# Kernel tuning notes

Hardware: AMD Instinct MI355X
Metric: run time of the kernel (lower is better)

The kernel has to match this reference:

```python
import jax, jax.numpy as jnp
import numpy as np

CH_IN, CH_OUT, CH, NLAYERS = 40, 9, 64, 10
CH_CLOSE = 2 * CH
KSZ = 9  # stencil hard-coded to 9 in init_weights
H = 0.1


def conv1(X, Ker):
    # F.conv1d(X, Ker, padding=(k-1)//2); Ker: (Cout, Cin, k)
    pad = (Ker.shape[-1] - 1) // 2
    return jax.lax.conv_general_dilated(X, Ker, (1,), [(pad, pad)],
                                        dimension_numbers=('NCH', 'OIH', 'NCH'))


def conv1T(X, Ker):
    # F.conv_transpose1d(X, Ker, padding=(k-1)//2) with stride 1 ==
    # conv1d with swapped in/out channels and flipped taps, padding k-1-(k-1)//2
    k = Ker.shape[-1]
    pad = k - 1 - (k - 1) // 2
    Kt = jnp.flip(jnp.swapaxes(Ker, 0, 1), -1)
    return jax.lax.conv_general_dilated(X, Kt, (1,), [(pad, pad)],
                                        dimension_numbers=('NCH', 'OIH', 'NCH'))


def mean_masked(X, mask, axis, keepdims=False):
    return jnp.sum(X * mask, axis=axis, keepdims=keepdims) / jnp.sum(mask, axis=axis, keepdims=keepdims)


def tr2dist(Y):
    # pairwise distances of columns of Y (B,C,N) -> (B,N,N), per Pfold tr2DistSmall
    k = Y.shape[1]
    Z = Y - jnp.mean(Y, axis=2, keepdims=True)
    n2 = jnp.sum(Z * Z, axis=1)  # (B,N)
    D = n2[:, :, None] + n2[:, None, :] - 2.0 * jnp.einsum('bcn,bcm->bnm', Z, Z)
    D = 3.0 * D / k
    Dr = jnp.maximum(D, 0.0)
    safe = jnp.where(Dr > 0, Dr, 1.0)  # grad-safe sqrt
    return jnp.where(Dr > 0, jnp.sqrt(safe), 0.0)


def get_graph_lap(X, mask, sigma):
    # X: (B,C,N), mask: (B,1,N)
    mm = jnp.einsum('bci,bcj->bij', mask, mask)  # (B,N,N) pair mask
    msum = jnp.sum(mask, axis=2, keepdims=True)
    Xc = X - (jnp.sum(X * mask, axis=2, keepdims=True) / msum) * mask
    Xc = Xc / jnp.sqrt(jnp.sum(Xc * Xc, axis=2, keepdims=True) / msum + 1e-4)
    N = X.shape[2]
    pos = 0.5 * jnp.linspace(0.0, 1.0, N)[None, None, :] * mask  # (B,1,N)
    Xa = jnp.concatenate([Xc, pos], axis=1)
    W = tr2dist(Xa) * mm
    W = jnp.exp(-W / sigma * 10.0) * mm
    Wsum = jnp.sum(W, axis=1)  # (B,N)
    D = Wsum[:, :, None] * jnp.eye(N, dtype=W.dtype)  # diag(Wsum)
    L = D - W
    return 0.5 * (L + jnp.swapaxes(L, 1, 2)), W


def double_sym(Z, Wi, Bi, L, mask):
    A0 = conv1(Z + Bi[0], Wi[0]) * mask
    A0 = (A0 - mean_masked(A0, mask, 2, True)) * mask
    A0 = A0 / jnp.sqrt(jnp.sum(A0 * A0, axis=1, keepdims=True) + 1e-3)
    A1 = (conv1(Z + Bi[1], Wi[1]) @ L) * mask
    A1 = (A1 - mean_masked(A1, mask, 2, True)) * mask
    A1 = A1 / jnp.sqrt(jnp.sum(A1 * A1, axis=1, keepdims=True) + 1e-3)
    A0 = jax.nn.relu(A0)
    A1 = jax.nn.relu(A1)
    A0 = conv1T(A0, Wi[0]) * mask
    A1 = (conv1T(A1, Wi[1]) @ L) * mask
    return A0 + A1


def hypernet_forward(Z, mask, Kopen, Kclose, W, Bias):
    mask = mask[:, None, :]  # (B,1,N)
    Z = jnp.einsum('ci,bin->bcn', Kopen, Z) * mask
    L, _ = get_graph_lap(Z, mask, 10.0)
    for i in range(W.shape[0]):
        if i % 10 == 0:
            L, _ = get_graph_lap(Z, mask, 10.0)
        Z = Z - H * double_sym(Z, W[i], Bias[i], L, mask)
    Z = jnp.einsum('oc,bcn->bon', Kclose, Z) * mask
    dists = jnp.stack([tr2dist(Z[:, 3 * i:3 * i + 3, :]) for i in range(Z.shape[1] // 3)], axis=1)
    return dists, Z  # dists: (B, chan_out//3, N, N)


def setup_inputs() -> dict:
    key = jax.random.key(0)
    ks = jax.random.split(key, 5)
    B, N = 8, 1024
    Z = jax.random.normal(ks[0], (B, CH_IN, N), dtype=jnp.float32)
    mask = jnp.ones((B, N), dtype=jnp.float32)
    so = float(CH) / CH_IN
    Kopen = jax.random.uniform(ks[1], (CH, CH_IN), minval=-so, maxval=so, dtype=jnp.float32)
    sc = float(CH_OUT) / CH
    Kclose = jax.random.uniform(ks[2], (CH_OUT, CH), minval=-sc, maxval=sc, dtype=jnp.float32)
    W = jax.random.uniform(ks[3], (NLAYERS, 2, CH_CLOSE, CH, KSZ), minval=-0.1, maxval=0.1, dtype=jnp.float32)
    Bias = jax.random.uniform(ks[4], (NLAYERS, 2, CH, 1), dtype=jnp.float32) * 0.001
    return {"Z": Z, "mask": mask, "Kopen": Kopen, "Kclose": Kclose, "W": W, "Bias": Bias}


def reference(Z, mask, Kopen, Kclose, W, Bias):
    return hypernet_forward(Z, mask, Kopen, Kclose, W, Bias)
```

## Files before the change

### kernel.cpp

```cpp
#include <hip/hip_runtime.h>
#include <cstddef>

#define BB 8
#define NN 1024
#define CIN 40
#define CH 64
#define CC 128
#define COUT 9
#define KS 9
#define NL 10
#define HSTEP 0.1f
#define SKC 2
#define SKH 4

typedef __attribute__((ext_vector_type(8))) short bf16x8;
typedef __attribute__((ext_vector_type(4))) float f32x4;

__device__ __forceinline__ unsigned short f2bf(float f) {
    union { float f; unsigned u; } v;
    v.f = f;
    unsigned u = v.u;
    u += 0x7FFFu + ((u >> 16) & 1u);
    return (unsigned short)(u >> 16);
}
__device__ __forceinline__ float bf2f(unsigned short h) {
    union { unsigned u; float f; } v;
    v.u = ((unsigned)h) << 16;
    return v.f;
}

__device__ __forceinline__ size_t pk_addr(int lb, int row, int col, int R, int KDv) {
    int chunk = ((lb * (R / 32) + (row >> 5)) * (KDv / 32) + (col >> 5)) * 2 + ((row >> 4) & 1);
    int lane = ((col >> 3) & 3) * 16 + (row & 15);
    return ((size_t)chunk * 64 + lane) * 8 + (col & 7);
}

__device__ __forceinline__ float blockSum(float v, float* red) {
    int tid = threadIdx.x;
    red[tid] = v;
    __syncthreads();
    for (int s = 128; s > 0; s >>= 1) {
        if (tid < s) red[tid] += red[tid + s];
        __syncthreads();
    }
    float r = red[0];
    __syncthreads();
    return r;
}

__global__ __launch_bounds__(256) void k_zero(float* __restrict__ p, int n) {
    int i = blockIdx.x * 256 + threadIdx.x;
    if (i < n) p[i] = 0.f;
}

__global__ __launch_bounds__(256) void k_prep_wbf(const float* __restrict__ Win,
                                                  unsigned short* __restrict__ PKc_h,
                                                  unsigned short* __restrict__ PKc_l,
                                                  unsigned short* __restrict__ PKt_h,
                                                  unsigned short* __restrict__ PKt_l) {
    int idx = blockIdx.x * 256 + threadIdx.x;
    const int total = NL * 2 * CC * CH * KS;
    if (idx >= total) return;
    int k = idx % KS;
    int t = idx / KS;
    int i = t % CH;  t /= CH;
    int o = t % CC;  t /= CC;
    int lb = t;
    float v = Win[idx];
    unsigned short h = f2bf(v);
    unsigned short l = f2bf(v - bf2f(h));
    size_t ac = pk_addr(lb, o, k * 64 + i, CC, 576);
    size_t at = pk_addr(lb, i, (8 - k) * 128 + o, CH, 1152);
    PKc_h[ac] = h;
    PKc_l[ac] = l;
    PKt_h[at] = h;
    PKt_l[at] = l;
}

__global__ __launch_bounds__(256) void k_prep_bks(const float* __restrict__ Win,
                                                  const float* __restrict__ Bias,
                                                  float* __restrict__ bks) {
    int idx = blockIdx.x * 256 + threadIdx.x;
    const int total = NL * 2 * CC * KS;
    if (idx >= total) return;
    int k = idx % KS;
    int t = idx / KS;
    int o = t % CC;
    int lb = t / CC;
    float s = 0.f;
    for (int i = 0; i < CH; ++i)
        s += Win[(((size_t)lb * CC + o) * CH + i) * KS + k] * Bias[lb * CH + i];
    bks[idx] = s;
}

__global__ __launch_bounds__(256) void k_open(const float* __restrict__ Zin,
                                              const float* __restrict__ mask,
                                              const float* __restrict__ Kop,
                                              float* __restrict__ Zcur) {
    int n = blockIdx.x * 256 + threadIdx.x;
    int c = blockIdx.y, b = blockIdx.z;
    float acc = 0.f;
    for (int i = 0; i < CIN; ++i)
        acc += Kop[c * CIN + i] * Zin[((size_t)b * CIN + i) * NN + n];
    Zcur[((size_t)b * CH + c) * NN + n] = acc * mask[b * NN + n];
}

__global__ __launch_bounds__(256) void k_za(const float* __restrict__ Zcur,
                                            const float* __restrict__ mask,
                                            float* __restrict__ Za) {
    __shared__ float red[256];
    int c = blockIdx.x;
    int b = blockIdx.y;
    int tid = threadIdx.x;
    const float* m = mask + b * NN;
    float x[4], mv[4];
    if (c < CH) {
        const float* src = Zcur + ((size_t)b * CH + c) * NN;
#pragma unroll
        for (int j = 0; j < 4; ++j) { int n = tid * 4 + j; x[j] = src[n]; mv[j] = m[n]; }
    } else {
#pragma unroll
        for (int j = 0; j < 4; ++j) { int n = tid * 4 + j; mv[j] = m[n]; x[j] = 0.5f * ((float)n / 1023.f) * mv[j]; }
    }
    float sm = 0.f, sxm = 0.f;
#pragma unroll
    for (int j = 0; j < 4; ++j) { sm += mv[j]; sxm += x[j] * mv[j]; }
    float msum = blockSum(sm, red);
    float xm = blockSum(sxm, red);
    if (c < CH) {
        float mean = xm / msum;
        float ss = 0.f;
#pragma unroll
        for (int j = 0; j < 4; ++j) { x[j] -= mean * mv[j]; ss += x[j] * x[j]; }
        ss = blockSum(ss, red);
        float sc = rsqrtf(ss / msum + 1e-4f);
#pragma unroll
        for (int j = 0; j < 4; ++j) x[j] *= sc;
    }
    float ps = 0.f;
#pragma unroll
    for (int j = 0; j < 4; ++j) ps += x[j];
    float pm = blockSum(ps, red) / (float)NN;
    float* dst = Za + ((size_t)b * 65 + c) * NN;
#pragma unroll
    for (int j = 0; j < 4; ++j) dst[tid * 4 + j] = x[j] - pm;
}

__global__ __launch_bounds__(256) void k_gramW(const float* __restrict__ Za,
                                               const float* __restrict__ mask,
                                               unsigned short* __restrict__ Wpk,
                                               float* __restrict__ Wsum) {
    __shared__ float As[65][68];
    __shared__ float Bs2[65][68];
    __shared__ unsigned short wt[64][72];
    __shared__ float csred[16][64];
    __shared__ float n2is[64], n2js[64];
    int i0 = blockIdx.x * 64, j0 = blockIdx.y * 64, b = blockIdx.z;
    int tid = threadIdx.x;
    for (int e = tid; e < 65 * 64; e += 256) {
        int c = e >> 6, t = e & 63;
        const float* src = Za + ((size_t)b * 65 + c) * NN;
        As[c][t] = src[i0 + t];
        Bs2[c][t] = src[j0 + t];
    }
    __syncthreads();
    if (tid < 64) {
        float s = 0.f;
        for (int c = 0; c < 65; ++c) { float v = As[c][tid]; s += v * v; }
        n2is[tid] = s;
    } else if (tid < 128) {
        int t = tid - 64;
        float s = 0.f;
        for (int c = 0; c < 65; ++c) { float v = Bs2[c][t]; s += v * v; }
        n2js[t] = s;
    }
    __syncthreads();
    int tx = tid & 15, ty = tid >> 4;
    float acc[4][4] = {};
    for (int c = 0; c < 65; ++c) {
        float a[4];
#pragma unroll
        for (int q = 0; q < 4; ++q) a[q] = As[c][ty * 4 + q];
        float bv[4];
        *reinterpret_cast<float4*>(bv) = *reinterpret_cast<const float4*>(&Bs2[c][tx * 4]);
#pragma unroll
        for (int q = 0; q < 4; ++q)
#pragma unroll
            for (int r = 0; r < 4; ++r) acc[q][r] += a[q] * bv[r];
    }
    const float* m = mask + b * NN;
    float csacc[4] = {0.f, 0.f, 0.f, 0.f};
    for (int q = 0; q < 4; ++q) {
        int i = i0 + ty * 4 + q;
        float n2i = n2is[ty * 4 + q], mi = m[i];
#pragma unroll
        for (int r = 0; r < 4; ++r) {
            int j = j0 + tx * 4 + r;
            float D = n2i + n2js[tx * 4 + r] - 2.f * acc[q][r];
            D *= (3.f / 65.f);
            D = fmaxf(D, 0.f);
            float dist = (D > 0.f) ? sqrtf(D) : 0.f;
            float mmv = mi * m[j];
            float res = expf(-dist * mmv) * mmv;
            wt[ty * 4 + q][tx * 4 + r] = f2bf(res);
            csacc[r] += res;
        }
    }
#pragma unroll
    for (int r = 0; r < 4; ++r) csred[ty][tx * 4 + r] = csacc[r];
    __syncthreads();
    for (int s = 8; s > 0; s >>= 1) {
        if (ty < s) {
#pragma unroll
            for (int r = 0; r < 4; ++r) csred[ty][tx * 4 + r] += csred[ty + s][tx * 4 + r];
        }
        __syncthreads();
    }
    if (ty == 0) {
#pragma unroll
        for (int r = 0; r < 4; ++r)
            atomicAdd(&Wsum[b * NN + j0 + tx * 4 + r], csred[0][tx * 4 + r]);
    }
    for (int e = tid; e < 512; e += 256) {
        int li = e >> 3, ljb = (e & 7) * 8;
        int row = i0 + li, col = j0 + ljb;
        int chunk = ((b * 32 + (row >> 5)) * 32 + (col >> 5)) * 2 + ((row >> 4) & 1);
        int lane2 = ((col >> 3) & 3) * 16 + (row & 15);
        unsigned short* dp = Wpk + ((size_t)chunk * 64 + lane2) * 8;
        *reinterpret_cast<ushort4*>(dp) = *reinterpret_cast<ushort4*>(&wt[li][ljb]);
        *reinterpret_cast<ushort4*>(dp + 4) = *reinterpret_cast<ushort4*>(&wt[li][ljb + 4]);
    }
}

__global__ __launch_bounds__(256) void k_conv1_mfma(const float* __restrict__ Zcur,
                                                    const unsigned short* __restrict__ Wh,
                                                    const unsigned short* __restrict__ Wl,
                                                    const float* __restrict__ bksl,
                                                    const float* __restrict__ mask,
                                                    float* __restrict__ C0,
                                                    float* __restrict__ C1,
                                                    unsigned short* __restrict__ C1pk) {
    __shared__ __align__(16) unsigned short xh[80][64];
    __shared__ __align__(16) unsigned short xl[80][64];
    int n0 = blockIdx.x * 64;
    int y = blockIdx.y;
    int b = blockIdx.z;
    int br = y >> 1, half = y & 1;
    int tid = threadIdx.x;
    const float* Xb = Zcur + (size_t)b * CH * NN;

    for (int e = tid; e < 64 * 20; e += 256) {
        int i = e / 20, t = e - i * 20;
        int gn = n0 + t * 4 - 4;
        float4 v = make_float4(0.f, 0.f, 0.f, 0.f);
        if (gn >= 0 && gn + 3 < NN) v = *reinterpret_cast<const float4*>(&Xb[(size_t)i * NN + gn]);
        float vv[4] = {v.x, v.y, v.z, v.w};
#pragma unroll
        for (int j = 0; j < 4; ++j) {
            int row = t * 4 + j;
            int col = i ^ ((row & 7) << 3);
            unsigned short h = f2bf(vv[j]);
            xh[row][col] = h;
            xl[row][col] = f2bf(vv[j] - bf2f(h));
        }
    }
    __syncthreads();

    int wid = tid >> 6, lane = tid & 63;
    int wo = (wid >> 1) * 32, wn = (wid & 1) * 32;
    int r = lane & 15, g = lane >> 4;
    int r32 = half * 2 + (wid >> 1);
    size_t brOff = (size_t)br * (CC / 32) * (576 / 32) * 1024;

    f32x4 acc[2][2] = {};
#pragma unroll 3
    for (int q = 0; q < 18; ++q) {
        int k = q >> 1, s = q & 1;
        size_t widx = brOff + ((size_t)(r32 * 18 + q)) * 1024 + lane * 8;
        bf16x8 ah[2], al[2];
        ah[0] = *reinterpret_cast<const bf16x8*>(&Wh[widx]);
        ah[1] = *reinterpret_cast<const bf16x8*>(&Wh[widx + 512]);
        al[0] = *reinterpret_cast<const bf16x8*>(&Wl[widx]);
        al[1] = *reinterpret_cast<const bf16x8*>(&Wl[widx + 512]);
        bf16x8 bh[2], bl[2];
#pragma unroll
        for (int fn = 0; fn < 2; ++fn) {
            int row = wn + fn * 16 + r + k;
            int chs = (s * 32 + g * 8) ^ ((row & 7) << 3);
            bh[fn] = *reinterpret_cast<const bf16x8*>(&xh[row][chs]);
            bl[fn] = *reinterpret_cast<const bf16x8*>(&xl[row][chs]);
        }
#pragma unroll
        for (int fc = 0; fc < 2; ++fc)
#pragma unroll
            for (int fn = 0; fn < 2; ++fn) {
                acc[fc][fn] = __builtin_amdgcn_mfma_f32_16x16x32_bf16(ah[fc], bh[fn], acc[fc][fn], 0, 0, 0);
                acc[fc][fn] = __builtin_amdgcn_mfma_f32_16x16x32_bf16(al[fc], bh[fn], acc[fc][fn], 0, 0, 0);
                acc[fc][fn] = __builtin_amdgcn_mfma_f32_16x16x32_bf16(ah[fc], bl[fn], acc[fc][fn], 0, 0, 0);
            }
    }

    const float* mkB = mask + b * NN;
    float* Outp = (br ? C1 : C0) + ((size_t)b * CC + half * 64) * NN;
    const float* bo_base = bksl + (br * CC + half * 64) * KS;
#pragma unroll
    for (int fc = 0; fc < 2; ++fc) {
#pragma unroll
        for (int fn = 0; fn < 2; ++fn) {
            int n = n0 + wn + fn * 16 + r;
#pragma unroll
            for (int rr = 0; rr < 4; ++rr) {
                int oo = wo + fc * 16 + 4 * g + rr;
                float v = acc[fc][fn][rr];
                const float* bo = bo_base + oo * KS;
                float bias = 0.f;
#pragma unroll
                for (int k = 0; k < KS; ++k) {
                    int nn2 = n + k - 4;
                    if (nn2 >= 0 && nn2 < NN) bias += bo[k];
                }
                v += bias;
                if (br == 0) v *= mkB[n];
                Outp[(size_t)oo * NN + n] = v;
                if (br == 1) {
                    int cg = half * 64 + oo;
                    int chunk = ((b * 4 + (cg >> 5)) * 32 + (n >> 5)) * 2 + ((cg >> 4) & 1);
                    int lane2 = ((n >> 3) & 3) * 16 + (cg & 15);
                    C1pk[((size_t)chunk * 64 + lane2) * 8 + (n & 7)] = f2bf(v);
                }
            }
        }
    }
}

__global__ __launch_bounds__(256) void k_convT_mfma(const float* __restrict__ C0,
                                                    const float* __restrict__ A1,
                                                    const unsigned short* __restrict__ Wh,
                                                    const unsigned short* __restrict__ Wl,
                                                    const float* __restrict__ mask,
                                                    const float* __restrict__ meanA,
                                                    float* __restrict__ T0,
                                                    float* __restrict__ T1p,
                                                    unsigned short* __restrict__ T1pk) {
    __shared__ float fs[48][132];
    __shared__ __align__(16) unsigned short xh[48][128];
    __shared__ __align__(16) unsigned short xl[48][128];
    __shared__ float red2[2][32][33];
    __shared__ float ps[48][4];
    __shared__ float invc[48];
    int n0 = blockIdx.x * 32;
    int br = blockIdx.y;
    int b = blockIdx.z;
    int tid = threadIdx.x;
    const float* Xb = (br ? A1 : C0) + (size_t)b * CC * NN;
    const float* meB = meanA + ((size_t)br * BB + b) * CC;
    const float* mkB = mask + b * NN;

    for (int e = tid; e < 128 * 12; e += 256) {
        int i = e / 12, t = e - i * 12;
        int gn = n0 + t * 4 - 4;
        float4 v = make_float4(0.f, 0.f, 0.f, 0.f);
        if (gn >= 0 && gn + 3 < NN) {
            v = *reinterpret_cast<const float4*>(&Xb[(size_t)i * NN + gn]);
            float me = meB[i];
            float4 mk = *reinterpret_cast<const float4*>(&mkB[gn]);
            v.x = (v.x - me) * mk.x;
            v.y = (v.y - me) * mk.y;
            v.z = (v.z - me) * mk.z;
            v.w = (v.w - me) * mk.w;
        }
        fs[t * 4 + 0][i] = v.x;
        fs[t * 4 + 1][i] = v.y;
        fs[t * 4 + 2][i] = v.z;
        fs[t * 4 + 3][i] = v.w;
    }
    __syncthreads();
    if (tid < 192) {
        int row = tid % 48, seg = tid / 48;
        float ss = 0.f;
#pragma unroll
        for (int i = 0; i < 32; ++i) { float v = fs[row][seg * 32 + i]; ss += v * v; }
        ps[row][seg] = ss;
    }
    __syncthreads();
    if (tid < 48) invc[tid] = rsqrtf(ps[tid][0] + ps[tid][1] + ps[tid][2] + ps[tid][3] + 0.001f);
    __syncthreads();
    for (int e = tid; e < 128 * 12; e += 256) {
        int i = e / 12, t = e - i * 12;
#pragma unroll
        for (int j = 0; j < 4; ++j) {
            int row = t * 4 + j;
            float v = fmaxf(fs[row][i] * invc[row], 0.f);
            int col = i ^ ((row & 7) << 3);
            unsigned short h = f2bf(v);
            xh[row][col] = h;
            xl[row][col] = f2bf(v - bf2f(h));
        }
    }
    __syncthreads();

    int wid = tid >> 6, lane = tid & 63;
    int i32 = wid & 1, kh = wid >> 1;
    int r = lane & 15, g = lane >> 4;
    size_t brW = (size_t)br * (CH / 32) * (1152 / 32) * 1024;

    f32x4 acc[2][2] = {};
#pragma unroll 3
    for (int t = 0; t < 18; ++t) {
        int k = t >> 1, s = kh * 2 + (t & 1);
        int q32 = k * 4 + s;
        size_t widx = brW + ((size_t)(i32 * 36 + q32)) * 1024 + lane * 8;
        bf16x8 ah[2], al[2];
        ah[0] = *reinterpret_cast<const bf16x8*>(&Wh[widx]);
        ah[1] = *reinterpret_cast<const bf16x8*>(&Wh[widx + 512]);
        al[0] = *reinterpret_cast<const bf16x8*>(&Wl[widx]);
        al[1] = *reinterpret_cast<const bf16x8*>(&Wl[widx + 512]);
        bf16x8 bh[2], bl[2];
#pragma unroll
        for (int fn = 0; fn < 2; ++fn) {
            int row = fn * 16 + r + k;
            int chs = (s * 32 + g * 8) ^ ((row & 7) << 3);
            bh[fn] = *reinterpret_cast<const bf16x8*>(&xh[row][chs]);
            bl[fn] = *reinterpret_cast<const bf16x8*>(&xl[row][chs]);
        }
#pragma unroll
        for (int fc = 0; fc < 2; ++fc)
#pragma unroll
            for (int fn = 0; fn < 2; ++fn) {
                acc[fc][fn] = __builtin_amdgcn_mfma_f32_16x16x32_bf16(ah[fc], bh[fn], acc[fc][fn], 0, 0, 0);
                acc[fc][fn] = __builtin_amdgcn_mfma_f32_16x16x32_bf16(al[fc], bh[fn], acc[fc][fn], 0, 0, 0);
                acc[fc][fn] = __builtin_amdgcn_mfma_f32_16x16x32_bf16(ah[fc], bl[fn], acc[fc][fn], 0, 0, 0);
            }
    }

    if (kh == 1) {
#pragma unroll
        for (int fc = 0; fc < 2; ++fc)
#pragma unroll
            for (int fn = 0; fn < 2; ++fn)
#pragma unroll
                for (int rr = 0; rr < 4; ++rr)
                    red2[i32][fc * 16 + 4 * g + rr][fn * 16 + r] = acc[fc][fn][rr];
    }
    __syncthreads();
    if (kh == 0) {
        float* Outp = (br ? T1p : T0) + (size_t)b * CH * NN;
#pragma unroll
        for (int fc = 0; fc < 2; ++fc)
#pragma unroll
            for (int fn = 0; fn < 2; ++fn) {
                int n = n0 + fn * 16 + r;
#pragma unroll
                for (int rr = 0; rr < 4; ++rr) {
                    int irow = fc * 16 + 4 * g + rr;
                    float v = acc[fc][fn][rr] + red2[i32][irow][fn * 16 + r];
                    Outp[(size_t)(i32 * 32 + irow) * NN + n] = v;
                    if (br == 1) {
                        int cg = i32 * 32 + irow;
                        int chunk = ((b * 2 + (cg >> 5)) * 32 + (n >> 5)) * 2 + ((cg >> 4) & 1);
                        int lane2 = ((n >> 3) & 3) * 16 + (cg & 15);
                        T1pk[((size_t)chunk * 64 + lane2) * 8 + (n & 7)] = f2bf(v);
                    }
                }
            }
    }
}

template <int SKN>
__global__ __launch_bounds__(256) void k_matL_mfma(const unsigned short* __restrict__ Xpk,
                                                   const unsigned short* __restrict__ Wpk,
                                                   float* __restrict__ Part, int rows) {
    int cb = rows >> 6;
    int sk = blockIdx.y;
    int b = blockIdx.z / cb;
    int c0 = (blockIdx.z % cb) * 64;
    int tid = threadIdx.x;
    int wid = tid >> 6, lane = tid & 63;
    int wc = (wid >> 1) * 32;
    int r = lane & 15, g = lane >> 4;
    int rowsT = rows >> 5;
    int ct = (c0 >> 5) + (wid >> 1);
    int nt32 = blockIdx.x * 2 + (wid & 1);
    const unsigned short* Xb = Xpk + ((size_t)(b * rowsT + ct)) * 32768 + (size_t)lane * 8;
    const unsigned short* Wb = Wpk + ((size_t)(b * 32 + nt32)) * 32768 + (size_t)lane * 8;

    f32x4 acc[2][2] = {};
    int ms_beg = sk * (32 / SKN);
#pragma unroll 4
    for (int ms = ms_beg; ms < ms_beg + 32 / SKN; ++ms) {
        bf16x8 a0 = *reinterpret_cast<const bf16x8*>(&Xb[(size_t)ms * 1024]);
        bf16x8 a1 = *reinterpret_cast<const bf16x8*>(&Xb[(size_t)ms * 1024 + 512]);
        bf16x8 w0 = *reinterpret_cast<const bf16x8*>(&Wb[(size_t)ms * 1024]);
        bf16x8 w1 = *reinterpret_cast<const bf16x8*>(&Wb[(size_t)ms * 1024 + 512]);
        acc[0][0] = __builtin_amdgcn_mfma_f32_16x16x32_bf16(a0, w0, acc[0][0], 0, 0, 0);
        acc[0][1] = __builtin_amdgcn_mfma_f32_16x16x32_bf16(a0, w1, acc[0][1], 0, 0, 0);
        acc[1][0] = __builtin_amdgcn_mfma_f32_16x16x32_bf16(a1, w0, acc[1][0], 0, 0, 0);
        acc[1][1] = __builtin_amdgcn_mfma_f32_16x16x32_bf16(a1, w1, acc[1][1], 0, 0, 0);
    }
    int n0 = blockIdx.x * 64;
    int wn = (wid & 1) * 32;
#pragma unroll
    for (int fc = 0; fc < 2; ++fc)
#pragma unroll
        for (int fn = 0; fn < 2; ++fn) {
            int ncol = n0 + wn + fn * 16 + r;
#pragma unroll
            for (int rr = 0; rr < 4; ++rr) {
                int crow = c0 + wc + fc * 16 + 4 * g + rr;
                Part[(((size_t)b * SKN + sk) * rows + crow) * NN + ncol] = acc[fc][fn][rr];
            }
        }
}

template <int SKN, int MODE>
__global__ __launch_bounds__(256) void k_matL_fin(const float* __restrict__ X,
                                                  const float* __restrict__ Part,
                                                  const float* __restrict__ Wsum,
                                                  const float* __restrict__ mask,
                                                  const float* __restrict__ T0,
                                                  float* __restrict__ Out,
                                                  float* __restrict__ meanA, int rows,
                                                  const float* __restrict__ C0p) {
    __shared__ float red[256];
    int c = blockIdx.x, b = blockIdx.y;
    int n = threadIdx.x * 4;
    float4 s = make_float4(0.f, 0.f, 0.f, 0.f);
#pragma unroll
    for (int sk = 0; sk < SKN; ++sk) {
        float4 p = *reinterpret_cast<const float4*>(
            &Part[(((size_t)b * SKN + sk) * rows + c) * NN + n]);
        s.x += p.x; s.y += p.y; s.z += p.z; s.w += p.w;
    }
    float4 xv = *reinterpret_cast<const float4*>(&X[((size_t)b * rows + c) * NN + n]);
    float4 wv = *reinterpret_cast<const float4*>(&Wsum[b * NN + n]);
    float4 mv = *reinterpret_cast<const float4*>(&mask[b * NN + n]);
    float y0 = xv.x * wv.x - s.x, y1 = xv.y * wv.y - s.y;
    float y2 = xv.z * wv.z - s.z, y3 = xv.w * wv.w - s.w;
    if (MODE == 0) {
        float4 res = make_float4(y0 * mv.x, y1 * mv.y, y2 * mv.z, y3 * mv.w);
        *reinterpret_cast<float4*>(&Out[((size_t)b * rows + c) * NN + n]) = res;
        float4 c0v = *reinterpret_cast<const float4*>(&C0p[((size_t)b * rows + c) * NN + n]);
        float rs = res.x * mv.x + res.y * mv.y + res.z * mv.z + res.w * mv.w;
        float cs = c0v.x * mv.x + c0v.y * mv.y + c0v.z * mv.z + c0v.w * mv.w;
        float ms = mv.x + mv.y + mv.z + mv.w;
        rs = blockSum(rs, red);
        cs = blockSum(cs, red);
        ms = blockSum(ms, red);
        if (threadIdx.x == 0) {
            meanA[(size_t)b * CC + c] = cs / ms;
            meanA[((size_t)BB + b) * CC + c] = rs / ms;
        }
    } else {
        float4 t0 = *reinterpret_cast<const float4*>(&T0[((size_t)b * rows + c) * NN + n]);
        float4 o = *reinterpret_cast<const float4*>(&Out[((size_t)b * rows + c) * NN + n]);
        float4 res = make_float4(o.x - HSTEP * mv.x * (t0.x + y0),
                                 o.y - HSTEP * mv.y * (t0.y + y1),
                                 o.z - HSTEP * mv.z * (t0.z + y2),
                                 o.w - HSTEP * mv.w * (t0.w + y3));
        *reinterpret_cast<float4*>(&Out[((size_t)b * rows + c) * NN + n]) = res;
    }
}

__global__ __launch_bounds__(256) void k_close(const float* __restrict__ Zcur,
                                               const float* __restrict__ Kcl,
                                               const float* __restrict__ mask,
                                               float* __restrict__ Zout) {
    __shared__ float red[4][64][COUT];
    int tid = threadIdx.x;
    int nl = tid & 63, cg = tid >> 6;
    int n = blockIdx.x * 64 + nl;
    int b = blockIdx.y;
    float acc[COUT] = {};
#pragma unroll
    for (int cc = 0; cc < 16; ++cc) {
        int c = cg * 16 + cc;
        float zv = Zcur[((size_t)b * CH + c) * NN + n];
#pragma unroll
        for (int o = 0; o < COUT; ++o) acc[o] += Kcl[o * CH + c] * zv;
    }
#pragma unroll
    for (int o = 0; o < COUT; ++o) red[cg][nl][o] = acc[o];
    __syncthreads();
    if (cg == 0) {
        float mv = mask[b * NN + n];
#pragma unroll
        for (int o = 0; o < COUT; ++o) {
            float s = red[0][nl][o] + red[1][nl][o] + red[2][nl][o] + red[3][nl][o];
            Zout[((size_t)b * COUT + o) * NN + n] = s * mv;
        }
    }
}

__global__ __launch_bounds__(256) void k_center3(const float* __restrict__ Zout, float* __restrict__ Zc3) {
    __shared__ float red[256];
    int c = blockIdx.x, b = blockIdx.y, tid = threadIdx.x;
    const float* src = Zout + ((size_t)b * COUT + c) * NN;
    float s = 0.f;
    for (int n = tid; n < NN; n += 256) s += src[n];
    float mean = blockSum(s, red) / (float)NN;
    float* dst = Zc3 + ((size_t)b * COUT + c) * NN;
    for (int n = tid; n < NN; n += 256) dst[n] = src[n] - mean;
}

__global__ __launch_bounds__(256) void k_dist(const float* __restrict__ Zc3,
                                              float* __restrict__ dout) {
    __shared__ float Ai[3][64], Aj[3][64], ni[64], nj[64];
    int bg = blockIdx.z;
    int b = bg / 3, g = bg - 3 * b;
    int i0 = blockIdx.x * 64, j0 = blockIdx.y * 64;
    int tid = threadIdx.x;
    for (int e = tid; e < 192; e += 256) {
        int c = e / 64, t = e - c * 64;
        Ai[c][t] = Zc3[((size_t)b * COUT + g * 3 + c) * NN + i0 + t];
    }
    for (int e = tid; e < 192; e += 256) {
        int c = e / 64, t = e - c * 64;
        Aj[c][t] = Zc3[((size_t)b * COUT + g * 3 + c) * NN + j0 + t];
    }
    __syncthreads();
    if (tid < 64) {
        ni[tid] = Ai[0][tid] * Ai[0][tid] + Ai[1][tid] * Ai[1][tid] + Ai[2][tid] * Ai[2][tid];
    } else if (tid < 128) {
        int t = tid - 64;
        nj[t] = Aj[0][t] * Aj[0][t] + Aj[1][t] * Aj[1][t] + Aj[2][t] * Aj[2][t];
    }
    __syncthreads();
    int tx = tid & 15, ty = tid >> 4;
    for (int q = 0; q < 4; ++q) {
        int i = ty * 4 + q;
        float a0 = Ai[0][i], a1 = Ai[1][i], a2 = Ai[2][i], n2i = ni[i];
        float res[4];
#pragma unroll
        for (int r = 0; r < 4; ++r) {
            int j = tx * 4 + r;
            float D = n2i + nj[j] - 2.f * (a0 * Aj[0][j] + a1 * Aj[1][j] + a2 * Aj[2][j]);
            D = fmaxf(D, 0.f);
            res[r] = (D > 0.f) ? sqrtf(D) : 0.f;
        }
        *reinterpret_cast<float4*>(&dout[(((size_t)b * 3 + g) * NN + i0 + i) * NN + j0 + tx * 4]) =
            *reinterpret_cast<float4*>(res);
    }
}

extern "C" void kernel_launch(void* const* d_in, const int* in_sizes, int n_in,
                              void* d_out, int out_size, void* d_ws, size_t ws_size,
                              hipStream_t stream) {
    (void)in_sizes; (void)n_in; (void)out_size; (void)ws_size;
    const float* Zin  = (const float*)d_in[0];
    const float* mask = (const float*)d_in[1];
    const float* Kop  = (const float*)d_in[2];
    const float* Kcl  = (const float*)d_in[3];
    const float* Win  = (const float*)d_in[4];
    const float* Bias = (const float*)d_in[5];
    float* out = (float*)d_out;
    float* ws = (float*)d_ws;

    size_t off = 0;
    float* Zcur = ws + off;  off += (size_t)BB * CH * NN;
    float* C0   = ws + off;  off += (size_t)BB * CC * NN;
    float* C1   = ws + off;  off += (size_t)BB * CC * NN;
    float* A1   = ws + off;  off += (size_t)BB * CC * NN;
    float* T0   = ws + off;  off += (size_t)BB * CH * NN;
    float* T1p  = ws + off;  off += (size_t)BB * CH * NN;
    float* Za   = ws + off;  off += (size_t)BB * 65 * NN;
    float* Wsum = ws + off;  off += (size_t)BB * NN;
    float* meanA= ws + off;  off += (size_t)2 * BB * CC;
    float* bks  = ws + off;  off += (size_t)NL * 2 * CC * KS;
    float* Zc3  = ws + off;  off += (size_t)BB * COUT * NN;

    float* Part = out;
    unsigned short* Wpk2  = (unsigned short*)(out + (size_t)4194304);
    unsigned short* C1pk  = (unsigned short*)(out + (size_t)8388608);
    unsigned short* T1pk  = (unsigned short*)(out + (size_t)8912896);
    unsigned short* PKc_h = (unsigned short*)(out + (size_t)14680064);
    unsigned short* PKc_l = (unsigned short*)(out + (size_t)15417344);
    unsigned short* PKt_h = (unsigned short*)(out + (size_t)16154624);
    unsigned short* PKt_l = (unsigned short*)(out + (size_t)16891904);

    const int wtot = NL * 2 * CC * CH * KS;
    k_prep_wbf<<<dim3((wtot + 255) / 256), 256, 0, stream>>>(Win, PKc_h, PKc_l, PKt_h, PKt_l);
    k_prep_bks<<<dim3((NL * 2 * CC * KS + 255) / 256), 256, 0, stream>>>(Win, Bias, bks);
    k_zero<<<dim3(BB * NN / 256), 256, 0, stream>>>(Wsum, BB * NN);
    k_open<<<dim3(NN / 256, CH, BB), 256, 0, stream>>>(Zin, mask, Kop, Zcur);
    k_za<<<dim3(65, BB), 256, 0, stream>>>(Zcur, mask, Za);
    k_gramW<<<dim3(16, 16, BB), 256, 0, stream>>>(Za, mask, Wpk2, Wsum);

    for (int l = 0; l < NL; ++l) {
        const unsigned short* PKc_h_l = PKc_h + (size_t)l * 2 * CC * 576;
        const unsigned short* PKc_l_l = PKc_l + (size_t)l * 2 * CC * 576;
        const unsigned short* PKt_h_l = PKt_h + (size_t)l * 2 * CH * 1152;
        const unsigned short* PKt_l_l = PKt_l + (size_t)l * 2 * CH * 1152;
        const float* bksl = bks + (size_t)l * 2 * CC * KS;

        k_conv1_mfma<<<dim3(NN / 64, 4, BB), 256, 0, stream>>>(
            Zcur, PKc_h_l, PKc_l_l, bksl, mask, C0, C1, C1pk);
        k_matL_mfma<SKC><<<dim3(NN / 64, SKC, BB * (CC / 64)), 256, 0, stream>>>(C1pk, Wpk2, Part, CC);
        k_matL_fin<SKC, 0><<<dim3(CC, BB), 256, 0, stream>>>(
            C1, Part, Wsum, mask, nullptr, A1, meanA, CC, C0);
        k_convT_mfma<<<dim3(NN / 32, 2, BB), 256, 0, stream>>>(
            C0, A1, PKt_h_l, PKt_l_l, mask, meanA, T0, T1p, T1pk);
        k_matL_mfma<SKH><<<dim3(NN / 64, SKH, BB * (CH / 64)), 256, 0, stream>>>(T1pk, Wpk2, Part, CH);
        k_matL_fin<SKH, 1><<<dim3(CH, BB), 256, 0, stream>>>(
            T1p, Part, Wsum, mask, T0, Zcur, nullptr, CH, nullptr);
    }

    float* Zout = out + (size_t)BB * 3 * NN * NN;
    k_close<<<dim3(NN / 64, BB), 256, 0, stream>>>(Zcur, Kcl, mask, Zout);
    k_center3<<<dim3(COUT, BB), 256, 0, stream>>>(Zout, Zc3);
    k_dist<<<dim3(16, 16, 3 * BB), 256, 0, stream>>>(Zc3, out);
}
```

Before: 817.7 us.

## Fuse graph-Laplacian matmul epilogues and move channel means into producer kernels

The split-K Laplacian matmul plus separate finalize kernel is replaced by one kernel per stage. Each of these kernels splits K across two wave pairs, reduces the partials in shared memory and applies the Wsum/mask epilogue directly, so the Part buffer no longer round-trips through global memory. Per-channel mean partial sums are now produced inside conv1 and the fused matmul kernel, and convT sums them at its start instead of relying on a block-reduction finalize pass. This removes two launches and a large intermediate per layer. The cost is a smaller grid with less K parallelism and extra partial-sum reads in convT.

```diff
diff --git a/kernel.cpp b/kernel.cpp
--- a/kernel.cpp
+++ b/kernel.cpp
@@ -10,8 +10,6 @@
 #define KS 9
 #define NL 10
 #define HSTEP 0.1f
-#define SKC 2
-#define SKH 4
 
 typedef __attribute__((ext_vector_type(8))) short bf16x8;
 typedef __attribute__((ext_vector_type(4))) float f32x4;
@@ -51,6 +49,16 @@
 __global__ __launch_bounds__(256) void k_zero(float* __restrict__ p, int n) {
     int i = blockIdx.x * 256 + threadIdx.x;
     if (i < n) p[i] = 0.f;
+}
+
+__global__ __launch_bounds__(256) void k_msum(const float* __restrict__ mask,
+                                              float* __restrict__ msum) {
+    __shared__ float red[256];
+    int b = blockIdx.x, tid = threadIdx.x;
+    float s = 0.f;
+    for (int n = tid; n < NN; n += 256) s += mask[b * NN + n];
+    s = blockSum(s, red);
+    if (tid == 0) msum[b] = s;
 }
 
 __global__ __launch_bounds__(256) void k_prep_wbf(const float* __restrict__ Win,
@@ -239,9 +247,11 @@
                                                     const float* __restrict__ mask,
                                                     float* __restrict__ C0,
                                                     float* __restrict__ C1,
-                                                    unsigned short* __restrict__ C1pk) {
+                                                    unsigned short* __restrict__ C1pk,
+                                                    float* __restrict__ meanP0) {
     __shared__ __align__(16) unsigned short xh[80][64];
     __shared__ __align__(16) unsigned short xl[80][64];
+    __shared__ float rs[64][2];
     int n0 = blockIdx.x * 64;
     int y = blockIdx.y;
     int b = blockIdx.z;
@@ -303,6 +313,7 @@
     const float* mkB = mask + b * NN;
     float* Outp = (br ? C1 : C0) + ((size_t)b * CC + half * 64) * NN;
     const float* bo_base = bksl + (br * CC + half * 64) * KS;
+    float p[2][4] = {};
 #pragma unroll
     for (int fc = 0; fc < 2; ++fc) {
 #pragma unroll
@@ -320,7 +331,10 @@
                     if (nn2 >= 0 && nn2 < NN) bias += bo[k];
                 }
                 v += bias;
-                if (br == 0) v *= mkB[n];
+                if (br == 0) {
+                    v *= mkB[n];
+                    p[fc][rr] += v * mkB[n];
+                }
                 Outp[(size_t)oo * NN + n] = v;
                 if (br == 1) {
                     int cg = half * 64 + oo;
@@ -331,6 +345,96 @@
             }
         }
     }
+    if (br == 0) {
+#pragma unroll
+        for (int fc = 0; fc < 2; ++fc)
+#pragma unroll
+            for (int rr = 0; rr < 4; ++rr) {
+                float v = p[fc][rr];
+                v += __shfl_xor(v, 1); v += __shfl_xor(v, 2);
+                v += __shfl_xor(v, 4); v += __shfl_xor(v, 8);
+                if (r == 0) rs[wo + fc * 16 + 4 * g + rr][wid & 1] = v;
+            }
+        __syncthreads();
+        if (tid < 64)
+            meanP0[((size_t)b * CC + half * 64 + tid) * 16 + blockIdx.x] = rs[tid][0] + rs[tid][1];
+    }
+}
+
+__global__ __launch_bounds__(256) void k_matL_cc(const unsigned short* __restrict__ C1pk,
+                                                 const unsigned short* __restrict__ Wpk,
+                                                 const float* __restrict__ C1,
+                                                 const float* __restrict__ Wsum,
+                                                 const float* __restrict__ mask,
+                                                 float* __restrict__ A1,
+                                                 float* __restrict__ meanP1) {
+    __shared__ float red2[2][32][33];
+    int nt32 = blockIdx.x;
+    int b = blockIdx.z >> 1, chalf = blockIdx.z & 1;
+    int c0 = chalf * 64;
+    int tid = threadIdx.x;
+    int wid = tid >> 6, lane = tid & 63;
+    int kh = wid >> 1, ch = wid & 1;
+    int r = lane & 15, g = lane >> 4;
+    int ct = chalf * 2 + ch;
+    const unsigned short* Xb = C1pk + ((size_t)(b * 4 + ct)) * 32768 + (size_t)lane * 8;
+    const unsigned short* Wb = Wpk + ((size_t)(b * 32 + nt32)) * 32768 + (size_t)lane * 8;
+
+    f32x4 acc[2][2] = {};
+#pragma unroll 4
+    for (int ms = kh * 16; ms < kh * 16 + 16; ++ms) {
+        bf16x8 a0 = *reinterpret_cast<const bf16x8*>(&Xb[(size_t)ms * 1024]);
+        bf16x8 a1 = *reinterpret_cast<const bf16x8*>(&Xb[(size_t)ms * 1024 + 512]);
+        bf16x8 w0 = *reinterpret_cast<const bf16x8*>(&Wb[(size_t)ms * 1024]);
+        bf16x8 w1 = *reinterpret_cast<const bf16x8*>(&Wb[(size_t)ms * 1024 + 512]);
+        acc[0][0] = __builtin_amdgcn_mfma_f32_16x16x32_bf16(a0, w0, acc[0][0], 0, 0, 0);
+        acc[0][1] = __builtin_amdgcn_mfma_f32_16x16x32_bf16(a0, w1, acc[0][1], 0, 0, 0);
+        acc[1][0] = __builtin_amdgcn_mfma_f32_16x16x32_bf16(a1, w0, acc[1][0], 0, 0, 0);
+        acc[1][1] = __builtin_amdgcn_mfma_f32_16x16x32_bf16(a1, w1, acc[1][1], 0, 0, 0);
+    }
+    if (kh == 1) {
+#pragma unroll
+        for (int fc = 0; fc < 2; ++fc)
+#pragma unroll
+            for (int fn = 0; fn < 2; ++fn)
+#pragma unroll
+                for (int rr = 0; rr < 4; ++rr)
+                    red2[ch][fc * 16 + 4 * g + rr][fn * 16 + r] = acc[fc][fn][rr];
+    }
+    __syncthreads();
+    if (kh == 0) {
+        const float* C1b = C1 + (size_t)b * CC * NN;
+        float* A1b = A1 + (size_t)b * CC * NN;
+        const float* mk = mask + b * NN;
+        const float* wsB = Wsum + b * NN;
+        float p[2][4] = {};
+#pragma unroll
+        for (int fc = 0; fc < 2; ++fc)
+#pragma unroll
+            for (int fn = 0; fn < 2; ++fn) {
+                int ncol = nt32 * 32 + fn * 16 + r;
+                float mkv = mk[ncol], wsv = wsB[ncol];
+#pragma unroll
+                for (int rr = 0; rr < 4; ++rr) {
+                    int crow = c0 + ch * 32 + fc * 16 + 4 * g + rr;
+                    float v = acc[fc][fn][rr] + red2[ch][fc * 16 + 4 * g + rr][fn * 16 + r];
+                    float y = C1b[(size_t)crow * NN + ncol] * wsv - v;
+                    float res = y * mkv;
+                    A1b[(size_t)crow * NN + ncol] = res;
+                    p[fc][rr] += res * mkv;
+                }
+            }
+#pragma unroll
+        for (int fc = 0; fc < 2; ++fc)
+#pragma unroll
+            for (int rr = 0; rr < 4; ++rr) {
+                float v = p[fc][rr];
+                v += __shfl_xor(v, 1); v += __shfl_xor(v, 2);
+                v += __shfl_xor(v, 4); v += __shfl_xor(v, 8);
+                if (r == 0)
+                    meanP1[((size_t)b * CC + c0 + ch * 32 + fc * 16 + 4 * g + rr) * 32 + nt32] = v;
+            }
+    }
 }
 
 __global__ __launch_bounds__(256) void k_convT_mfma(const float* __restrict__ C0,
@@ -338,7 +442,9 @@
                                                     const unsigned short* __restrict__ Wh,
                                                     const unsigned short* __restrict__ Wl,
                                                     const float* __restrict__ mask,
-                                                    const float* __restrict__ meanA,
+                                                    const float* __restrict__ meanP0,
+                                                    const float* __restrict__ meanP1,
+                                                    const float* __restrict__ msum,
                                                     float* __restrict__ T0,
                                                     float* __restrict__ T1p,
                                                     unsigned short* __restrict__ T1pk) {
@@ -348,13 +454,28 @@
     __shared__ float red2[2][32][33];
     __shared__ float ps[48][4];
     __shared__ float invc[48];
+    __shared__ float meB_sh[128];
     int n0 = blockIdx.x * 32;
     int br = blockIdx.y;
     int b = blockIdx.z;
     int tid = threadIdx.x;
     const float* Xb = (br ? A1 : C0) + (size_t)b * CC * NN;
-    const float* meB = meanA + ((size_t)br * BB + b) * CC;
     const float* mkB = mask + b * NN;
+
+    if (tid < 128) {
+        float s = 0.f;
+        if (br == 0) {
+            const float* mp = meanP0 + ((size_t)b * CC + tid) * 16;
+#pragma unroll
+            for (int t = 0; t < 16; ++t) s += mp[t];
+        } else {
+            const float* mp = meanP1 + ((size_t)b * CC + tid) * 32;
+#pragma unroll
+            for (int t = 0; t < 32; ++t) s += mp[t];
+        }
+        meB_sh[tid] = s / msum[b];
+    }
+    __syncthreads();
 
     for (int e = tid; e < 128 * 12; e += 256) {
         int i = e / 12, t = e - i * 12;
@@ -362,7 +483,7 @@
         float4 v = make_float4(0.f, 0.f, 0.f, 0.f);
         if (gn >= 0 && gn + 3 < NN) {
             v = *reinterpret_cast<const float4*>(&Xb[(size_t)i * NN + gn]);
-            float me = meB[i];
+            float me = meB_sh[i];
             float4 mk = *reinterpret_cast<const float4*>(&mkB[gn]);
             v.x = (v.x - me) * mk.x;
             v.y = (v.y - me) * mk.y;
@@ -466,28 +587,26 @@
     }
 }
 
-template <int SKN>
-__global__ __launch_bounds__(256) void k_matL_mfma(const unsigned short* __restrict__ Xpk,
-                                                   const unsigned short* __restrict__ Wpk,
-                                                   float* __restrict__ Part, int rows) {
-    int cb = rows >> 6;
-    int sk = blockIdx.y;
-    int b = blockIdx.z / cb;
-    int c0 = (blockIdx.z % cb) * 64;
+__global__ __launch_bounds__(256) void k_matL_ch(const unsigned short* __restrict__ T1pk,
+                                                 const unsigned short* __restrict__ Wpk,
+                                                 const float* __restrict__ T1p,
+                                                 const float* __restrict__ Wsum,
+                                                 const float* __restrict__ mask,
+                                                 const float* __restrict__ T0,
+                                                 float* __restrict__ Zcur) {
+    __shared__ float red2[2][32][33];
+    int nt32 = blockIdx.x;
+    int b = blockIdx.z;
     int tid = threadIdx.x;
     int wid = tid >> 6, lane = tid & 63;
-    int wc = (wid >> 1) * 32;
+    int kh = wid >> 1, ch = wid & 1;
     int r = lane & 15, g = lane >> 4;
-    int rowsT = rows >> 5;
-    int ct = (c0 >> 5) + (wid >> 1);
-    int nt32 = blockIdx.x * 2 + (wid & 1);
-    const unsigned short* Xb = Xpk + ((size_t)(b * rowsT + ct)) * 32768 + (size_t)lane * 8;
+    const unsigned short* Xb = T1pk + ((size_t)(b * 2 + ch)) * 32768 + (size_t)lane * 8;
     const unsigned short* Wb = Wpk + ((size_t)(b * 32 + nt32)) * 32768 + (size_t)lane * 8;
 
     f32x4 acc[2][2] = {};
-    int ms_beg = sk * (32 / SKN);
 #pragma unroll 4
-    for (int ms = ms_beg; ms < ms_beg + 32 / SKN; ++ms) {
+    for (int ms = kh * 16; ms < kh * 16 + 16; ++ms) {
         bf16x8 a0 = *reinterpret_cast<const bf16x8*>(&Xb[(size_t)ms * 1024]);
         bf16x8 a1 = *reinterpret_cast<const bf16x8*>(&Xb[(size_t)ms * 1024 + 512]);
         bf16x8 w0 = *reinterpret_cast<const bf16x8*>(&Wb[(size_t)ms * 1024]);
@@ -497,67 +616,37 @@
         acc[1][0] = __builtin_amdgcn_mfma_f32_16x16x32_bf16(a1, w0, acc[1][0], 0, 0, 0);
         acc[1][1] = __builtin_amdgcn_mfma_f32_16x16x32_bf16(a1, w1, acc[1][1], 0, 0, 0);
     }
-    int n0 = blockIdx.x * 64;
-    int wn = (wid & 1) * 32;
-#pragma unroll
-    for (int fc = 0; fc < 2; ++fc)
-#pragma unroll
-        for (int fn = 0; fn < 2; ++fn) {
-            int ncol = n0 + wn + fn * 16 + r;
-#pragma unroll
-            for (int rr = 0; rr < 4; ++rr) {
-                int crow = c0 + wc + fc * 16 + 4 * g + rr;
-                Part[(((size_t)b * SKN + sk) * rows + crow) * NN + ncol] = acc[fc][fn][rr];
+    if (kh == 1) {
+#pragma unroll
+        for (int fc = 0; fc < 2; ++fc)
+#pragma unroll
+            for (int fn = 0; fn < 2; ++fn)
+#pragma unroll
+                for (int rr = 0; rr < 4; ++rr)
+                    red2[ch][fc * 16 + 4 * g + rr][fn * 16 + r] = acc[fc][fn][rr];
+    }
+    __syncthreads();
+    if (kh == 0) {
+        const float* T1b = T1p + (size_t)b * CH * NN;
+        const float* T0b = T0 + (size_t)b * CH * NN;
+        float* Zb = Zcur + (size_t)b * CH * NN;
+        const float* mk = mask + b * NN;
+        const float* wsB = Wsum + b * NN;
+#pragma unroll
+        for (int fc = 0; fc < 2; ++fc)
+#pragma unroll
+            for (int fn = 0; fn < 2; ++fn) {
+                int ncol = nt32 * 32 + fn * 16 + r;
+                float mkv = mk[ncol], wsv = wsB[ncol];
+#pragma unroll
+                for (int rr = 0; rr < 4; ++rr) {
+                    int crow = ch * 32 + fc * 16 + 4 * g + rr;
+                    float v = acc[fc][fn][rr] + red2[ch][fc * 16 + 4 * g + rr][fn * 16 + r];
+                    float y = T1b[(size_t)crow * NN + ncol] * wsv - v;
+                    size_t zi = (size_t)crow * NN + ncol;
+                    Zb[zi] = Zb[zi] - HSTEP * mkv * (T0b[zi] + y);
+                }
             }
-        }
-}
-
-template <int SKN, int MODE>
-__global__ __launch_bounds__(256) void k_matL_fin(const float* __restrict__ X,
-                                                  const float* __restrict__ Part,
-                                                  const float* __restrict__ Wsum,
-                                                  const float* __restrict__ mask,
-                                                  const float* __restrict__ T0,
-                                                  float* __restrict__ Out,
-                                                  float* __restrict__ meanA, int rows,
-                                                  const float* __restrict__ C0p) {
-    __shared__ float red[256];
-    int c = blockIdx.x, b = blockIdx.y;
-    int n = threadIdx.x * 4;
-    float4 s = make_float4(0.f, 0.f, 0.f, 0.f);
-#pragma unroll
-    for (int sk = 0; sk < SKN; ++sk) {
-        float4 p = *reinterpret_cast<const float4*>(
-            &Part[(((size_t)b * SKN + sk) * rows + c) * NN + n]);
-        s.x += p.x; s.y += p.y; s.z += p.z; s.w += p.w;
-    }
-    float4 xv = *reinterpret_cast<const float4*>(&X[((size_t)b * rows + c) * NN + n]);
-    float4 wv = *reinterpret_cast<const float4*>(&Wsum[b * NN + n]);
-    float4 mv = *reinterpret_cast<const float4*>(&mask[b * NN + n]);
-    float y0 = xv.x * wv.x - s.x, y1 = xv.y * wv.y - s.y;
-    float y2 = xv.z * wv.z - s.z, y3 = xv.w * wv.w - s.w;
-    if (MODE == 0) {
-        float4 res = make_float4(y0 * mv.x, y1 * mv.y, y2 * mv.z, y3 * mv.w);
-        *reinterpret_cast<float4*>(&Out[((size_t)b * rows + c) * NN + n]) = res;
-        float4 c0v = *reinterpret_cast<const float4*>(&C0p[((size_t)b * rows + c) * NN + n]);
-        float rs = res.x * mv.x + res.y * mv.y + res.z * mv.z + res.w * mv.w;
-        float cs = c0v.x * mv.x + c0v.y * mv.y + c0v.z * mv.z + c0v.w * mv.w;
-        float ms = mv.x + mv.y + mv.z + mv.w;
-        rs = blockSum(rs, red);
-        cs = blockSum(cs, red);
-        ms = blockSum(ms, red);
-        if (threadIdx.x == 0) {
-            meanA[(size_t)b * CC + c] = cs / ms;
-            meanA[((size_t)BB + b) * CC + c] = rs / ms;
-        }
-    } else {
-        float4 t0 = *reinterpret_cast<const float4*>(&T0[((size_t)b * rows + c) * NN + n]);
-        float4 o = *reinterpret_cast<const float4*>(&Out[((size_t)b * rows + c) * NN + n]);
-        float4 res = make_float4(o.x - HSTEP * mv.x * (t0.x + y0),
-                                 o.y - HSTEP * mv.y * (t0.y + y1),
-                                 o.z - HSTEP * mv.z * (t0.z + y2),
-                                 o.w - HSTEP * mv.w * (t0.w + y3));
-        *reinterpret_cast<float4*>(&Out[((size_t)b * rows + c) * NN + n]) = res;
     }
 }
 
@@ -664,11 +753,12 @@
     float* T1p  = ws + off;  off += (size_t)BB * CH * NN;
     float* Za   = ws + off;  off += (size_t)BB * 65 * NN;
     float* Wsum = ws + off;  off += (size_t)BB * NN;
-    float* meanA= ws + off;  off += (size_t)2 * BB * CC;
     float* bks  = ws + off;  off += (size_t)NL * 2 * CC * KS;
     float* Zc3  = ws + off;  off += (size_t)BB * COUT * NN;
-
-    float* Part = out;
+    float* meanP0 = ws + off; off += (size_t)BB * CC * 16;
+    float* meanP1 = ws + off; off += (size_t)BB * CC * 32;
+    float* msum = ws + off;  off += (size_t)BB;
+
     unsigned short* Wpk2  = (unsigned short*)(out + (size_t)4194304);
     unsigned short* C1pk  = (unsigned short*)(out + (size_t)8388608);
     unsigned short* T1pk  = (unsigned short*)(out + (size_t)8912896);
@@ -681,6 +771,7 @@
     k_prep_wbf<<<dim3((wtot + 255) / 256), 256, 0, stream>>>(Win, PKc_h, PKc_l, PKt_h, PKt_l);
     k_prep_bks<<<dim3((NL * 2 * CC * KS + 255) / 256), 256, 0, stream>>>(Win, Bias, bks);
     k_zero<<<dim3(BB * NN / 256), 256, 0, stream>>>(Wsum, BB * NN);
+    k_msum<<<dim3(BB), 256, 0, stream>>>(mask, msum);
     k_open<<<dim3(NN / 256, CH, BB), 256, 0, stream>>>(Zin, mask, Kop, Zcur);
     k_za<<<dim3(65, BB), 256, 0, stream>>>(Zcur, mask, Za);
     k_gramW<<<dim3(16, 16, BB), 256, 0, stream>>>(Za, mask, Wpk2, Wsum);
@@ -693,15 +784,13 @@
         const float* bksl = bks + (size_t)l * 2 * CC * KS;
 
         k_conv1_mfma<<<dim3(NN / 64, 4, BB), 256, 0, stream>>>(
-            Zcur, PKc_h_l, PKc_l_l, bksl, mask, C0, C1, C1pk);
-        k_matL_mfma<SKC><<<dim3(NN / 64, SKC, BB * (CC / 64)), 256, 0, stream>>>(C1pk, Wpk2, Part, CC);
-        k_matL_fin<SKC, 0><<<dim3(CC, BB), 256, 0, stream>>>(
-            C1, Part, Wsum, mask, nullptr, A1, meanA, CC, C0);
+            Zcur, PKc_h_l, PKc_l_l, bksl, mask, C0, C1, C1pk, meanP0);
+        k_matL_cc<<<dim3(NN / 32, 1, BB * 2), 256, 0, stream>>>(
+            C1pk, Wpk2, C1, Wsum, mask, A1, meanP1);
         k_convT_mfma<<<dim3(NN / 32, 2, BB), 256, 0, stream>>>(
-            C0, A1, PKt_h_l, PKt_l_l, mask, meanA, T0, T1p, T1pk);
-        k_matL_mfma<SKH><<<dim3(NN / 64, SKH, BB * (CH / 64)), 256, 0, stream>>>(T1pk, Wpk2, Part, CH);
-        k_matL_fin<SKH, 1><<<dim3(CH, BB), 256, 0, stream>>>(
-            T1p, Part, Wsum, mask, T0, Zcur, nullptr, CH, nullptr);
+            C0, A1, PKt_h_l, PKt_l_l, mask, meanP0, meanP1, msum, T0, T1p, T1pk);
+        k_matL_ch<<<dim3(NN / 32, 1, BB), 256, 0, stream>>>(
+            T1pk, Wpk2, T1p, Wsum, mask, T0, Zcur);
     }
 
     float* Zout = out + (size_t)BB * 3 * NN * NN;
```

Result: faster. 773.4 us (median of 2 runs) (-5.4%).
